# Optimization experiments

Hardware: AMD Instinct MI355X
Metric: run time of the kernel (lower is better)

The kernel has to match this reference:

```python
import jax, jax.numpy as jnp
import numpy as np

TEMP_EPS = 1e-6


def setup_inputs() -> dict:
    key = jax.random.key(0)
    k1, k2, k3 = jax.random.split(key, 3)
    B, V = 128, 128256
    logits = jax.random.normal(k1, (B, V), dtype=jnp.float32)
    temperatures = jax.random.uniform(k2, (B,), dtype=jnp.float32)
    u = jax.random.uniform(k3, (B, V), dtype=jnp.float32)
    return {"logits": logits, "temperatures": temperatures, "u": u}


def reference(logits, temperatures, u):
    # Faithful vectorized version of the per-row loop:
    #   nan_to_num -> temperature scale -> softmax -> multinomial sample,
    # expressed as a single Gumbel-max over the batch (equivalent sampling
    # distribution), with greedy argmax where temp <= 1e-6.
    logits = jnp.nan_to_num(logits)                       # [B, V]
    greedy = jnp.argmax(logits, axis=-1)                  # [B]

    safe_temp = jnp.maximum(temperatures, TEMP_EPS)[:, None]  # [B, 1]
    scaled = logits / safe_temp                           # [B, V]

    # Gumbel-max trick: argmax(scaled + g), g ~ Gumbel(0,1), samples
    # exactly from softmax(scaled) == the multinomial in the original.
    uc = jnp.clip(u, 1e-10, 1.0 - 1e-7)
    gumbel = -jnp.log(-jnp.log(uc))                       # [B, V]
    sampled = jnp.argmax(scaled + gumbel, axis=-1)        # [B]

    use_greedy = temperatures <= TEMP_EPS                 # [B] bool
    return jnp.where(use_greedy, greedy, sampled)
```

## Files before the change

### kernel.cpp

```cpp
#include <hip/hip_runtime.h>
#include <cfloat>
#include <cstdint>


#define TEMP_EPS 1e-6f

static constexpr int V      = 128256;
static constexpr int V4     = V / 4;
static constexpr int SEGS   = 16;
static constexpr int SEG_V4 = V4 / SEGS;

__device__ __forceinline__ float nan_to_num_f(float x) {
    if (x != x) return 0.0f;
    if (fabsf(x) == INFINITY) return x > 0.0f ? FLT_MAX : -FLT_MAX;
    return x;
}

__device__ __forceinline__ unsigned long long pack_key(float v, int idx) {
    unsigned u = __float_as_uint(v);
    u = (u & 0x80000000u) ? ~u : (u | 0x80000000u);
    return ((unsigned long long)u << 32) | (unsigned)(~(unsigned)idx);
}

__device__ __forceinline__ unsigned long long umax64(unsigned long long a,
                                                     unsigned long long b) {
    return a > b ? a : b;
}

__global__ __launch_bounds__(256) void sampler_partial_kernel(
    const float* __restrict__ logits,
    const float* __restrict__ temps,
    const float* __restrict__ u,
    unsigned long long* __restrict__ partials) {
    const int row = blockIdx.y;
    const int seg = blockIdx.x;

    const float temp = temps[row];
    const bool greedy = (temp <= TEMP_EPS);
    const float safe_temp = fmaxf(temp, TEMP_EPS);

    const float4* __restrict__ l4 = (const float4*)(logits + (size_t)row * V);
    const float4* __restrict__ u4 = (const float4*)(u + (size_t)row * V);

    const float UC_LO = 1e-10f;
    const float UC_HI = (float)(1.0 - 1e-7);

    unsigned long long key = 0ULL;

    const int seg_begin = seg * SEG_V4;
    const int seg_end   = seg_begin + SEG_V4;

    if (greedy) {
        for (int i = seg_begin + threadIdx.x; i < seg_end; i += 256) {
            float4 lv = l4[i];
            const int base = i * 4;
            float a = nan_to_num_f(lv.x);
            float b = nan_to_num_f(lv.y);
            float c = nan_to_num_f(lv.z);
            float d = nan_to_num_f(lv.w);
            key = umax64(key, pack_key(a, base + 0));
            key = umax64(key, pack_key(b, base + 1));
            key = umax64(key, pack_key(c, base + 2));
            key = umax64(key, pack_key(d, base + 3));
        }
    } else {
        for (int i = seg_begin + threadIdx.x; i < seg_end; i += 256) {
            float4 lv = l4[i];
            float4 uv = u4[i];
            const int base = i * 4;

            float l0 = nan_to_num_f(lv.x) / safe_temp;
            float l1 = nan_to_num_f(lv.y) / safe_temp;
            float l2 = nan_to_num_f(lv.z) / safe_temp;
            float l3 = nan_to_num_f(lv.w) / safe_temp;

            float c0 = fminf(fmaxf(uv.x, UC_LO), UC_HI);
            float c1 = fminf(fmaxf(uv.y, UC_LO), UC_HI);
            float c2 = fminf(fmaxf(uv.z, UC_LO), UC_HI);
            float c3 = fminf(fmaxf(uv.w, UC_LO), UC_HI);

            float g0 = -__logf(-__logf(c0));
            float g1 = -__logf(-__logf(c1));
            float g2 = -__logf(-__logf(c2));
            float g3 = -__logf(-__logf(c3));
            g0 = -logf(-logf(c0));
            g1 = -logf(-logf(c1));
            g2 = -logf(-logf(c2));
            g3 = -logf(-logf(c3));

            key = umax64(key, pack_key(l0 + g0, base + 0));
            key = umax64(key, pack_key(l1 + g1, base + 1));
            key = umax64(key, pack_key(l2 + g2, base + 2));
            key = umax64(key, pack_key(l3 + g3, base + 3));
        }
    }

    for (int o = 32; o > 0; o >>= 1)
        key = umax64(key, __shfl_down(key, o));

    __shared__ unsigned long long sdata[4];
    if ((threadIdx.x & 63) == 0) sdata[threadIdx.x >> 6] = key;
    __syncthreads();

    if (threadIdx.x == 0) {
        for (int w = 1; w < 4; ++w) key = umax64(key, sdata[w]);
        partials[row * SEGS + seg] = key;
    }
}

__global__ __launch_bounds__(64) void sampler_reduce_kernel(
    const unsigned long long* __restrict__ partials,
    int* __restrict__ out) {
    const int row = blockIdx.x;
    const int t = threadIdx.x;
    unsigned long long key = (t < SEGS) ? partials[row * SEGS + t] : 0ULL;
    for (int o = 32; o > 0; o >>= 1)
        key = umax64(key, __shfl_down(key, o));
    if (t == 0)
        out[row] = (int)(~(unsigned)(key & 0xFFFFFFFFull));
}

extern "C" void kernel_launch(void* const* d_in, const int* in_sizes, int n_in,
                              void* d_out, int out_size, void* d_ws, size_t ws_size,
                              hipStream_t stream) {
    const float* logits = (const float*)d_in[0];
    const float* temps  = (const float*)d_in[1];
    const float* u      = (const float*)d_in[2];
    int* out = (int*)d_out;
    const int B = in_sizes[1];

    unsigned long long* partials = (unsigned long long*)d_ws;

    dim3 grid1(SEGS, B);
    hipLaunchKernelGGL(sampler_partial_kernel, grid1, dim3(256), 0, stream,
                       logits, temps, u, partials);
    hipLaunchKernelGGL(sampler_reduce_kernel, dim3(B), dim3(64), 0, stream,
                       partials, out);
}
```

Baseline: 153.3 us.

## Double segments per row and issue all loads up front with fixed unrolled work

Result: faster. 148.6 us (-3.1%).

```diff
diff --git a/kernel.cpp b/kernel.cpp
--- a/kernel.cpp
+++ b/kernel.cpp
@@ -5,21 +5,22 @@
 
 #define TEMP_EPS 1e-6f
 
-static constexpr int V      = 128256;
-static constexpr int V4     = V / 4;
-static constexpr int SEGS   = 16;
-static constexpr int SEG_V4 = V4 / SEGS;
+static constexpr int V       = 128256;
+static constexpr int V4      = V / 4;
+static constexpr int SEGS    = 32;
+static constexpr int SEG_V4  = V4 / SEGS;
+static constexpr int TAIL    = SEG_V4 - 3 * 256;
 
 __device__ __forceinline__ float nan_to_num_f(float x) {
     if (x != x) return 0.0f;
-    if (fabsf(x) == INFINITY) return x > 0.0f ? FLT_MAX : -FLT_MAX;
-    return x;
+    return fminf(fmaxf(x, -FLT_MAX), FLT_MAX);
 }
 
 __device__ __forceinline__ unsigned long long pack_key(float v, int idx) {
-    unsigned u = __float_as_uint(v);
-    u = (u & 0x80000000u) ? ~u : (u | 0x80000000u);
-    return ((unsigned long long)u << 32) | (unsigned)(~(unsigned)idx);
+    unsigned b = __float_as_uint(v);
+    unsigned mask = (unsigned)(((int)b >> 31)) | 0x80000000u;
+    b ^= mask;
+    return ((unsigned long long)b << 32) | (unsigned)(~(unsigned)idx);
 }
 
 __device__ __forceinline__ unsigned long long umax64(unsigned long long a,
@@ -34,6 +35,7 @@
     unsigned long long* __restrict__ partials) {
     const int row = blockIdx.y;
     const int seg = blockIdx.x;
+    const int tid = threadIdx.x;
 
     const float temp = temps[row];
     const bool greedy = (temp <= TEMP_EPS);
@@ -45,53 +47,59 @@
     const float UC_LO = 1e-10f;
     const float UC_HI = (float)(1.0 - 1e-7);
 
+    const int base = seg * SEG_V4;
+
+    int idx[4];
+    idx[0] = base + tid;
+    idx[1] = base + 256 + tid;
+    idx[2] = base + 512 + tid;
+    idx[3] = (tid < TAIL) ? (base + 768 + tid) : (base + tid);
+
+    float4 lv[4], uv[4];
+#pragma unroll
+    for (int k = 0; k < 4; ++k) lv[k] = l4[idx[k]];
+#pragma unroll
+    for (int k = 0; k < 4; ++k) uv[k] = u4[idx[k]];
+
     unsigned long long key = 0ULL;
 
-    const int seg_begin = seg * SEG_V4;
-    const int seg_end   = seg_begin + SEG_V4;
-
     if (greedy) {
-        for (int i = seg_begin + threadIdx.x; i < seg_end; i += 256) {
-            float4 lv = l4[i];
-            const int base = i * 4;
-            float a = nan_to_num_f(lv.x);
-            float b = nan_to_num_f(lv.y);
-            float c = nan_to_num_f(lv.z);
-            float d = nan_to_num_f(lv.w);
-            key = umax64(key, pack_key(a, base + 0));
-            key = umax64(key, pack_key(b, base + 1));
-            key = umax64(key, pack_key(c, base + 2));
-            key = umax64(key, pack_key(d, base + 3));
+#pragma unroll
+        for (int k = 0; k < 4; ++k) {
+            const int e = idx[k] * 4;
+            float a = nan_to_num_f(lv[k].x);
+            float b = nan_to_num_f(lv[k].y);
+            float c = nan_to_num_f(lv[k].z);
+            float d = nan_to_num_f(lv[k].w);
+            key = umax64(key, pack_key(a, e + 0));
+            key = umax64(key, pack_key(b, e + 1));
+            key = umax64(key, pack_key(c, e + 2));
+            key = umax64(key, pack_key(d, e + 3));
         }
     } else {
-        for (int i = seg_begin + threadIdx.x; i < seg_end; i += 256) {
-            float4 lv = l4[i];
-            float4 uv = u4[i];
-            const int base = i * 4;
+#pragma unroll
+        for (int k = 0; k < 4; ++k) {
+            const int e = idx[k] * 4;
 
-            float l0 = nan_to_num_f(lv.x) / safe_temp;
-            float l1 = nan_to_num_f(lv.y) / safe_temp;
-            float l2 = nan_to_num_f(lv.z) / safe_temp;
-            float l3 = nan_to_num_f(lv.w) / safe_temp;
+            float l0 = nan_to_num_f(lv[k].x) / safe_temp;
+            float l1 = nan_to_num_f(lv[k].y) / safe_temp;
+            float l2 = nan_to_num_f(lv[k].z) / safe_temp;
+            float l3 = nan_to_num_f(lv[k].w) / safe_temp;
 
-            float c0 = fminf(fmaxf(uv.x, UC_LO), UC_HI);
-            float c1 = fminf(fmaxf(uv.y, UC_LO), UC_HI);
-            float c2 = fminf(fmaxf(uv.z, UC_LO), UC_HI);
-            float c3 = fminf(fmaxf(uv.w, UC_LO), UC_HI);
+            float c0 = fminf(fmaxf(uv[k].x, UC_LO), UC_HI);
+            float c1 = fminf(fmaxf(uv[k].y, UC_LO), UC_HI);
+            float c2 = fminf(fmaxf(uv[k].z, UC_LO), UC_HI);
+            float c3 = fminf(fmaxf(uv[k].w, UC_LO), UC_HI);
 
-            float g0 = -__logf(-__logf(c0));
-            float g1 = -__logf(-__logf(c1));
-            float g2 = -__logf(-__logf(c2));
-            float g3 = -__logf(-__logf(c3));
-            g0 = -logf(-logf(c0));
-            g1 = -logf(-logf(c1));
-            g2 = -logf(-logf(c2));
-            g3 = -logf(-logf(c3));
+            float g0 = -logf(-logf(c0));
+            float g1 = -logf(-logf(c1));
+            float g2 = -logf(-logf(c2));
+            float g3 = -logf(-logf(c3));
 
-            key = umax64(key, pack_key(l0 + g0, base + 0));
-            key = umax64(key, pack_key(l1 + g1, base + 1));
-            key = umax64(key, pack_key(l2 + g2, base + 2));
-            key = umax64(key, pack_key(l3 + g3, base + 3));
+            key = umax64(key, pack_key(l0 + g0, e + 0));
+            key = umax64(key, pack_key(l1 + g1, e + 1));
+            key = umax64(key, pack_key(l2 + g2, e + 2));
+            key = umax64(key, pack_key(l3 + g3, e + 3));
         }
     }
 
@@ -99,10 +107,10 @@
         key = umax64(key, __shfl_down(key, o));
 
     __shared__ unsigned long long sdata[4];
-    if ((threadIdx.x & 63) == 0) sdata[threadIdx.x >> 6] = key;
+    if ((tid & 63) == 0) sdata[tid >> 6] = key;
     __syncthreads();
 
-    if (threadIdx.x == 0) {
+    if (tid == 0) {
         for (int w = 1; w < 4; ++w) key = umax64(key, sdata[w]);
         partials[row * SEGS + seg] = key;
     }
```

## Double-buffer logits and uniforms into LDS via async global_load_lds

Applied to the files above, without the earlier changes.

Result: no change. 152.8 us (-0.3%).

```diff
diff --git a/kernel.cpp b/kernel.cpp
--- a/kernel.cpp
+++ b/kernel.cpp
@@ -9,17 +9,18 @@
 static constexpr int V4     = V / 4;
 static constexpr int SEGS   = 16;
 static constexpr int SEG_V4 = V4 / SEGS;
+static constexpr int CHUNKS = (SEG_V4 + 255) / 256;
 
 __device__ __forceinline__ float nan_to_num_f(float x) {
     if (x != x) return 0.0f;
-    if (fabsf(x) == INFINITY) return x > 0.0f ? FLT_MAX : -FLT_MAX;
-    return x;
+    return fminf(fmaxf(x, -FLT_MAX), FLT_MAX);
 }
 
 __device__ __forceinline__ unsigned long long pack_key(float v, int idx) {
-    unsigned u = __float_as_uint(v);
-    u = (u & 0x80000000u) ? ~u : (u | 0x80000000u);
-    return ((unsigned long long)u << 32) | (unsigned)(~(unsigned)idx);
+    unsigned b = __float_as_uint(v);
+    unsigned mask = (unsigned)(((int)b >> 31)) | 0x80000000u;
+    b ^= mask;
+    return ((unsigned long long)b << 32) | (unsigned)(~(unsigned)idx);
 }
 
 __device__ __forceinline__ unsigned long long umax64(unsigned long long a,
@@ -27,17 +28,36 @@
     return a > b ? a : b;
 }
 
+template <int IMM>
+__device__ __forceinline__ void wait_raw() { __builtin_amdgcn_s_waitcnt(IMM); }
+static constexpr int WAIT_VM2 = 0x0F72;
+static constexpr int WAIT_VM0 = 0x0F70;
+
+__device__ __forceinline__ void async_f4(const float4* gsrc, float4* lds_base) {
+    __builtin_amdgcn_global_load_lds(
+        (const __attribute__((address_space(1))) unsigned int*)gsrc,
+        (__attribute__((address_space(3))) unsigned int*)lds_base,
+        16, 0, 0);
+}
+
 __global__ __launch_bounds__(256) void sampler_partial_kernel(
     const float* __restrict__ logits,
     const float* __restrict__ temps,
     const float* __restrict__ u,
     unsigned long long* __restrict__ partials) {
-    const int row = blockIdx.y;
-    const int seg = blockIdx.x;
+    __shared__ float4 sL[2][256];
+    __shared__ float4 sU[2][256];
+    __shared__ unsigned long long sdata[4];
+
+    const int row  = blockIdx.y;
+    const int seg  = blockIdx.x;
+    const int tid  = threadIdx.x;
+    const int wave = tid >> 6;
 
     const float temp = temps[row];
     const bool greedy = (temp <= TEMP_EPS);
     const float safe_temp = fmaxf(temp, TEMP_EPS);
+    const float inv_temp = 1.0f / safe_temp;
 
     const float4* __restrict__ l4 = (const float4*)(logits + (size_t)row * V);
     const float4* __restrict__ u4 = (const float4*)(u + (size_t)row * V);
@@ -45,64 +65,72 @@
     const float UC_LO = 1e-10f;
     const float UC_HI = (float)(1.0 - 1e-7);
 
+    const int base    = seg * SEG_V4;
+    const int seg_end = base + SEG_V4;
+
+    auto f4_of = [&](int c) {
+        int f = base + c * 256 + tid;
+        return (f < seg_end) ? f : (base + tid);
+    };
+
+    auto stage = [&](int c, int slot) {
+        const int f = f4_of(c);
+        async_f4(l4 + f, &sL[slot][wave * 64]);
+        async_f4(u4 + f, &sU[slot][wave * 64]);
+    };
+
     unsigned long long key = 0ULL;
 
-    const int seg_begin = seg * SEG_V4;
-    const int seg_end   = seg_begin + SEG_V4;
+    auto compute = [&](int c, int slot) {
+        const int f = f4_of(c);
+        const float4 lv = sL[slot][tid];
+        const float4 uv = sU[slot][tid];
+        const int e = f * 4;
 
-    if (greedy) {
-        for (int i = seg_begin + threadIdx.x; i < seg_end; i += 256) {
-            float4 lv = l4[i];
-            const int base = i * 4;
-            float a = nan_to_num_f(lv.x);
-            float b = nan_to_num_f(lv.y);
-            float c = nan_to_num_f(lv.z);
-            float d = nan_to_num_f(lv.w);
-            key = umax64(key, pack_key(a, base + 0));
-            key = umax64(key, pack_key(b, base + 1));
-            key = umax64(key, pack_key(c, base + 2));
-            key = umax64(key, pack_key(d, base + 3));
-        }
-    } else {
-        for (int i = seg_begin + threadIdx.x; i < seg_end; i += 256) {
-            float4 lv = l4[i];
-            float4 uv = u4[i];
-            const int base = i * 4;
+        float x0 = nan_to_num_f(lv.x);
+        float x1 = nan_to_num_f(lv.y);
+        float x2 = nan_to_num_f(lv.z);
+        float x3 = nan_to_num_f(lv.w);
 
-            float l0 = nan_to_num_f(lv.x) / safe_temp;
-            float l1 = nan_to_num_f(lv.y) / safe_temp;
-            float l2 = nan_to_num_f(lv.z) / safe_temp;
-            float l3 = nan_to_num_f(lv.w) / safe_temp;
+        float c0 = fminf(fmaxf(uv.x, UC_LO), UC_HI);
+        float c1 = fminf(fmaxf(uv.y, UC_LO), UC_HI);
+        float c2 = fminf(fmaxf(uv.z, UC_LO), UC_HI);
+        float c3 = fminf(fmaxf(uv.w, UC_LO), UC_HI);
 
-            float c0 = fminf(fmaxf(uv.x, UC_LO), UC_HI);
-            float c1 = fminf(fmaxf(uv.y, UC_LO), UC_HI);
-            float c2 = fminf(fmaxf(uv.z, UC_LO), UC_HI);
-            float c3 = fminf(fmaxf(uv.w, UC_LO), UC_HI);
+        float g0 = -__logf(-logf(c0));
+        float g1 = -__logf(-logf(c1));
+        float g2 = -__logf(-logf(c2));
+        float g3 = -__logf(-logf(c3));
 
-            float g0 = -__logf(-__logf(c0));
-            float g1 = -__logf(-__logf(c1));
-            float g2 = -__logf(-__logf(c2));
-            float g3 = -__logf(-__logf(c3));
-            g0 = -logf(-logf(c0));
-            g1 = -logf(-logf(c1));
-            g2 = -logf(-logf(c2));
-            g3 = -logf(-logf(c3));
+        float v0 = greedy ? x0 : x0 * inv_temp + g0;
+        float v1 = greedy ? x1 : x1 * inv_temp + g1;
+        float v2 = greedy ? x2 : x2 * inv_temp + g2;
+        float v3 = greedy ? x3 : x3 * inv_temp + g3;
 
-            key = umax64(key, pack_key(l0 + g0, base + 0));
-            key = umax64(key, pack_key(l1 + g1, base + 1));
-            key = umax64(key, pack_key(l2 + g2, base + 2));
-            key = umax64(key, pack_key(l3 + g3, base + 3));
-        }
+        unsigned long long k0 = pack_key(v0, e + 0);
+        unsigned long long k1 = pack_key(v1, e + 1);
+        unsigned long long k2 = pack_key(v2, e + 2);
+        unsigned long long k3 = pack_key(v3, e + 3);
+        key = umax64(key, umax64(umax64(k0, k1), umax64(k2, k3)));
+    };
+
+    stage(0, 0);
+    stage(1, 1);
+#pragma unroll
+    for (int c = 0; c < CHUNKS; ++c) {
+        if (c < CHUNKS - 1) wait_raw<WAIT_VM2>();
+        else                wait_raw<WAIT_VM0>();
+        compute(c, c & 1);
+        if (c + 2 < CHUNKS) stage(c + 2, c & 1);
     }
 
     for (int o = 32; o > 0; o >>= 1)
         key = umax64(key, __shfl_down(key, o));
 
-    __shared__ unsigned long long sdata[4];
-    if ((threadIdx.x & 63) == 0) sdata[threadIdx.x >> 6] = key;
+    if ((tid & 63) == 0) sdata[wave] = key;
     __syncthreads();
 
-    if (threadIdx.x == 0) {
+    if (tid == 0) {
         for (int w = 1; w < 4; ++w) key = umax64(key, sdata[w]);
         partials[row * SEGS + seg] = key;
     }
```
